# Kernel tuning notes

Measured on AMD Instinct MI355X. Metric: run time of the kernel, lower is better.

The kernel has to match this reference:

```python
import jax, jax.numpy as jnp
import numpy as np

HIDDEN = 1024
N_HEADS = 16
N_KV = 4
HEAD_DIM = HIDDEN // N_HEADS  # 64


def setup_inputs() -> dict:
    key = jax.random.key(0)
    ks = jax.random.split(key, 10)
    B, S, D = 2, 2048, HIDDEN
    s = 0.02
    return {
        "hidden_states": jax.random.normal(ks[0], (B, S, D), jnp.float32),
        "attention_mask": jnp.ones((B, S), jnp.float32),
        "Wq": jax.random.normal(ks[1], (D, N_HEADS * HEAD_DIM), jnp.float32) * s,
        "bq": jnp.zeros((N_HEADS * HEAD_DIM,), jnp.float32),
        "Wk": jax.random.normal(ks[2], (D, N_KV * HEAD_DIM), jnp.float32) * s,
        "bk": jnp.zeros((N_KV * HEAD_DIM,), jnp.float32),
        "Wv": jax.random.normal(ks[3], (D, N_KV * HEAD_DIM), jnp.float32) * s,
        "bv": jnp.zeros((N_KV * HEAD_DIM,), jnp.float32),
        "Wo": jax.random.normal(ks[4], (D, D), jnp.float32) * s,
        "bo": jnp.zeros((D,), jnp.float32),
    }


def _rope(x):
    # x: [B, H, S, Dh]; half-split RoPE as in the torch module
    S, Dh = x.shape[-2], x.shape[-1]
    inv_freq = 1.0 / (10000.0 ** (jnp.arange(0, Dh, 2, dtype=jnp.float32) / Dh))
    freqs = jnp.arange(S, dtype=jnp.float32)[:, None] * inv_freq[None, :]  # [S, Dh/2]
    cos, sin = jnp.cos(freqs), jnp.sin(freqs)
    x1, x2 = jnp.split(x, 2, axis=-1)
    return jnp.concatenate([x1 * cos - x2 * sin, x1 * sin + x2 * cos], axis=-1)


def reference(hidden_states, attention_mask, Wq, bq, Wk, bk, Wv, bv, Wo, bo):
    B, S, D = hidden_states.shape
    q = (hidden_states @ Wq + bq).reshape(B, S, N_HEADS, HEAD_DIM).transpose(0, 2, 1, 3)
    k = (hidden_states @ Wk + bk).reshape(B, S, N_KV, HEAD_DIM).transpose(0, 2, 1, 3)
    v = (hidden_states @ Wv + bv).reshape(B, S, N_KV, HEAD_DIM).transpose(0, 2, 1, 3)
    q = _rope(q)
    k = _rope(k)
    rep = N_HEADS // N_KV
    k = jnp.repeat(k, rep, axis=1)  # [B, H, S, Dh]
    v = jnp.repeat(v, rep, axis=1)
    bias = (1.0 - attention_mask[:, None, None, :]) * -1e9  # [B,1,1,S]
    scores = jnp.einsum("bhqd,bhkd->bhqk", q, k) / jnp.sqrt(jnp.float32(HEAD_DIM))
    attn = jax.nn.softmax(scores + bias, axis=-1)
    out = jnp.einsum("bhqk,bhkd->bhqd", attn, v)
    out = out.transpose(0, 2, 1, 3).reshape(B, S, D)
    return out @ Wo + bo
```

## Files before the change

### kernel.cpp

```cpp
#include <hip/hip_runtime.h>

typedef __bf16 bf16;
typedef __attribute__((ext_vector_type(8))) __bf16 bf16x8;
typedef __attribute__((ext_vector_type(4))) __bf16 bf16x4;
typedef __attribute__((ext_vector_type(4))) float f32x4;
typedef __attribute__((ext_vector_type(16))) float f32x16;
typedef __attribute__((ext_vector_type(4))) unsigned int uint4v;

#define LOG2E 1.44269504088896340736f
#define QSCALE 0.18033688011112042f

__device__ inline void tr_tile(const float* __restrict__ in, bf16* __restrict__ out,
                               int R, int C, int bx, int by, int tid) {
    __shared__ float t[32][33];
    int tx = tid & 31, ty = tid >> 5;
    int rbase = by * 32, cbase = bx * 32;
#pragma unroll
    for (int i = 0; i < 4; i++) {
        int r = ty + i * 8;
        t[r][tx] = in[(size_t)(rbase + r) * C + cbase + tx];
    }
    __syncthreads();
#pragma unroll
    for (int i = 0; i < 4; i++) {
        int r = ty + i * 8;
        out[(size_t)(cbase + r) * R + rbase + tx] = (bf16)t[tx][r];
    }
}

__global__ __launch_bounds__(256) void prep_k(const float* __restrict__ X,
                                              const float* __restrict__ Wq,
                                              const float* __restrict__ Wk,
                                              const float* __restrict__ Wv,
                                              const float* __restrict__ Wo,
                                              const float* __restrict__ mask,
                                              bf16* __restrict__ Xb,
                                              bf16* __restrict__ WqT,
                                              bf16* __restrict__ WkT,
                                              bf16* __restrict__ WvT,
                                              bf16* __restrict__ WoT,
                                              float2* __restrict__ rt,
                                              float* __restrict__ Mb,
                                              int* __restrict__ mflags) {
    int blk = blockIdx.x, tid = threadIdx.x;
    if (blk < 2048) {
        int idx = (blk * 256 + tid) * 8;
        float4 a = *(const float4*)(X + idx);
        float4 b = *(const float4*)(X + idx + 4);
        bf16 v[8] = {(bf16)a.x, (bf16)a.y, (bf16)a.z, (bf16)a.w,
                     (bf16)b.x, (bf16)b.y, (bf16)b.z, (bf16)b.w};
        *(uint4*)(Xb + idx) = *(const uint4*)v;
    } else if (blk < 3072) {
        int t = blk - 2048; tr_tile(Wq, WqT, 1024, 1024, t & 31, t >> 5, tid);
    } else if (blk < 3328) {
        int t = blk - 3072; tr_tile(Wk, WkT, 1024, 256, t & 7, t >> 3, tid);
    } else if (blk < 3584) {
        int t = blk - 3328; tr_tile(Wv, WvT, 1024, 256, t & 7, t >> 3, tid);
    } else if (blk < 4608) {
        int t = blk - 3584; tr_tile(Wo, WoT, 1024, 1024, t & 31, t >> 5, tid);
    } else if (blk < 4864) {
        int idx = (blk - 4608) * 256 + tid;
        int s = idx >> 5, i = idx & 31;
        float inv = exp2f(-0.41524100370589830f * (float)i);
        float ang = (float)s * inv;
        rt[idx] = make_float2(cosf(ang), sinf(ang));
    } else {
        __shared__ int sflag;
        int b = blk - 4864;
        if (tid == 0) sflag = 1;
        __syncthreads();
        const float* mrow = mask + (size_t)b * 2048;
        int i0 = tid * 8;
        bool ones = true;
#pragma unroll
        for (int j = 0; j < 8; j++) {
            float m = mrow[i0 + j];
            if (m != 1.0f) ones = false;
            Mb[(size_t)b * 2048 + i0 + j] = (1.0f - m) * (-1e9f) * LOG2E;
        }
        if (!ones) sflag = 0;
        __syncthreads();
        if (tid == 0) mflags[b] = sflag;
    }
}

__global__ __launch_bounds__(256) void vtrans_k(const unsigned short* __restrict__ in,
                                                unsigned short* __restrict__ out) {
    __shared__ unsigned short t[32][33];
    int z = blockIdx.z;
    const unsigned short* ip = in + (size_t)z * 2048 * 64;
    unsigned short* op = out + (size_t)z * 2048 * 64;
    int tx = threadIdx.x & 31, ty = threadIdx.x >> 5;
    int rbase = blockIdx.y * 32, cbase = blockIdx.x * 32;
#pragma unroll
    for (int i = 0; i < 4; i++) {
        int r = ty + i * 8;
        t[r][tx] = ip[(size_t)(rbase + r) * 64 + cbase + tx];
    }
    __syncthreads();
#pragma unroll
    for (int i = 0; i < 4; i++) {
        int r = ty + i * 8;
        op[(size_t)(cbase + r) * 2048 + rbase + tx] = t[tx][r];
    }
}

__device__ __forceinline__ void gemm_main_12864(const bf16* __restrict__ A,
                                                const bf16* __restrict__ BT,
                                                int m0, int n0, int tid,
                                                f32x4 (&acc)[2][4]) {
    __shared__ bf16 As[128 * 64];
    __shared__ bf16 Bs[64 * 64];
    int w = tid >> 6, lane = tid & 63, l15 = lane & 15, quad = lane >> 4;

    int srow = lane >> 3;
    int kx = ((lane & 7) ^ srow) * 8;
    const bf16* ga0 = A + (size_t)(m0 + w * 32 + srow) * 1024 + kx;
    const bf16* gb0 = BT + (size_t)(n0 + w * 16 + srow) * 1024 + kx;
    bf16* la0 = As + (w * 32) * 64 + lane * 8;
    bf16* lb0 = Bs + (w * 16) * 64 + lane * 8;

    for (int k0 = 0; k0 < 1024; k0 += 64) {
#pragma unroll
        for (int p = 0; p < 4; p++)
            __builtin_amdgcn_global_load_lds(
                (const __attribute__((address_space(1))) unsigned int*)(ga0 + (size_t)p * 8 * 1024 + k0),
                (__attribute__((address_space(3))) unsigned int*)(la0 + p * 512), 16, 0, 0);
#pragma unroll
        for (int p = 0; p < 2; p++)
            __builtin_amdgcn_global_load_lds(
                (const __attribute__((address_space(1))) unsigned int*)(gb0 + (size_t)p * 8 * 1024 + k0),
                (__attribute__((address_space(3))) unsigned int*)(lb0 + p * 512), 16, 0, 0);
        __syncthreads();
#pragma unroll
        for (int half = 0; half < 2; half++) {
            bf16x8 a[2], bfr[4];
            int kp = ((half * 4 + quad) ^ (l15 & 7)) * 8;
#pragma unroll
            for (int i = 0; i < 2; i++)
                a[i] = *(const bf16x8*)&As[(w * 32 + i * 16 + l15) * 64 + kp];
#pragma unroll
            for (int j = 0; j < 4; j++)
                bfr[j] = *(const bf16x8*)&Bs[(j * 16 + l15) * 64 + kp];
#pragma unroll
            for (int i = 0; i < 2; i++)
#pragma unroll
                for (int j = 0; j < 4; j++)
                    acc[i][j] = __builtin_amdgcn_mfma_f32_16x16x32_bf16(a[i], bfr[j], acc[i][j], 0, 0, 0);
        }
        __syncthreads();
    }
}

__global__ __launch_bounds__(256) void qkv_gemm2(const bf16* __restrict__ Xb,
                                                 const bf16* __restrict__ WTall,
                                                 const float* __restrict__ bq,
                                                 const float* __restrict__ bk,
                                                 const float* __restrict__ bv,
                                                 const float2* __restrict__ rt,
                                                 bf16* __restrict__ Qb,
                                                 bf16* __restrict__ Kb,
                                                 bf16* __restrict__ Vb) {
    int tt = blockIdx.x, gy = blockIdx.y, tid = threadIdx.x;
    f32x4 acc[2][4] = {};
    gemm_main_12864(Xb, WTall, tt * 128, gy * 64, tid, acc);

    int w = tid >> 6, lane = tid & 63, l15 = lane & 15, quad = lane >> 4;
    const float* bias;
    bf16* dst;
    int mode, head;
    if (gy < 16)      { head = gy;      bias = bq + head * 64; dst = Qb; mode = 0; }
    else if (gy < 20) { head = gy - 16; bias = bk + head * 64; dst = Kb; mode = 1; }
    else              { head = gy - 20; bias = bv + head * 64; dst = Vb; mode = 2; }

#pragma unroll
    for (int i = 0; i < 2; i++) {
#pragma unroll
        for (int r = 0; r < 4; r++) {
            int token = tt * 128 + w * 32 + i * 16 + quad * 4 + r;
            int b = token >> 11, s = token & 2047;
            float vals[4];
#pragma unroll
            for (int j = 0; j < 4; j++) vals[j] = acc[i][j][r] + bias[j * 16 + l15];
            if (mode <= 1) {
#pragma unroll
                for (int c = 0; c < 2; c++) {
                    float2 cs2 = rt[s * 32 + c * 16 + l15];
                    float x1 = vals[c], x2 = vals[c + 2];
                    vals[c]     = x1 * cs2.x - x2 * cs2.y;
                    vals[c + 2] = x1 * cs2.y + x2 * cs2.x;
                }
            }
            if (mode == 0) {
#pragma unroll
                for (int j = 0; j < 4; j++) vals[j] *= QSCALE;
            }
            size_t base;
            if (mode == 0) base = (((size_t)b * 16 + head) * 2048 + s) * 64;
            else           base = (((size_t)b * 4  + head) * 2048 + s) * 64;
#pragma unroll
            for (int j = 0; j < 4; j++) dst[base + j * 16 + l15] = (bf16)vals[j];
        }
    }
}

__global__ __launch_bounds__(256) void oproj_gemm2(const bf16* __restrict__ Ab,
                                                   const bf16* __restrict__ WoT,
                                                   const float* __restrict__ bo,
                                                   float* __restrict__ out) {
    int tt = blockIdx.x, nt = blockIdx.y, tid = threadIdx.x;
    f32x4 acc[2][4] = {};
    gemm_main_12864(Ab, WoT, tt * 128, nt * 64, tid, acc);

    int w = tid >> 6, lane = tid & 63, l15 = lane & 15, quad = lane >> 4;
#pragma unroll
    for (int i = 0; i < 2; i++) {
#pragma unroll
        for (int r = 0; r < 4; r++) {
            int token = tt * 128 + w * 32 + i * 16 + quad * 4 + r;
#pragma unroll
            for (int j = 0; j < 4; j++) {
                int n = nt * 64 + j * 16 + l15;
                out[(size_t)token * 1024 + n] = acc[i][j][r] + bo[n];
            }
        }
    }
}

__global__ __launch_bounds__(256, 4) void attn_k(const bf16* __restrict__ Qb,
                                                 const bf16* __restrict__ Kb,
                                                 const bf16* __restrict__ VbT,
                                                 const float* __restrict__ Mb,
                                                 const int* __restrict__ mflags,
                                                 bf16* __restrict__ Opb,
                                                 float* __restrict__ Lp) {
    int qt = blockIdx.x, h = blockIdx.y, z = blockIdx.z;
    int b = z >> 1, sp = z & 1;
    int kvh = h >> 2;
    int kt0 = sp * 16;

    __shared__ bf16 Ks[2][64 * 64];
    __shared__ bf16 Vs[2][64 * 64];

    int tid = threadIdx.x, w = tid >> 6, lane = tid & 63, l31 = lane & 31, hi = lane >> 5;

    const bool maskOnes = (mflags[b] != 0);

    bf16x8 qa[4];
    {
        size_t qrow = (((size_t)b * 16 + h) * 2048 + (size_t)qt * 128 + w * 32 + l31) * 64;
#pragma unroll
        for (int ds = 0; ds < 4; ds++)
            qa[ds] = *(const bf16x8*)(Qb + qrow + ds * 16 + hi * 8);
    }

    f32x16 oacc[2] = {};
    float lsum = 0.f;

    size_t kRow = ((size_t)b * 4 + kvh) * 2048;
    size_t vRow = ((size_t)b * 4 + kvh) * 64;

    int srow = lane >> 3;
    int kx = ((lane & 7) ^ srow) * 8;
    const bf16* gk0 = Kb + (kRow + w * 16 + srow) * 64 + kx;
    const bf16* gv0 = VbT + (vRow + w * 16 + srow) * 2048 + kx;
    int lofs = (w * 16) * 64 + lane * 8;

#define STAGE(KT, BUF)                                                                              \
    do {                                                                                            \
        _Pragma("unroll")                                                                           \
        for (int p = 0; p < 2; p++) {                                                               \
            __builtin_amdgcn_global_load_lds(                                                       \
                (const __attribute__((address_space(1))) unsigned int*)(gk0 + ((size_t)(KT) * 64 + p * 8) * 64), \
                (__attribute__((address_space(3))) unsigned int*)(&Ks[BUF][0] + lofs + p * 512), 16, 0, 0); \
            __builtin_amdgcn_global_load_lds(                                                       \
                (const __attribute__((address_space(1))) unsigned int*)(gv0 + (size_t)p * 8 * 2048 + (KT) * 64), \
                (__attribute__((address_space(3))) unsigned int*)(&Vs[BUF][0] + lofs + p * 512), 16, 0, 0); \
        }                                                                                           \
    } while (0)

    STAGE(kt0, 0);
    __syncthreads();

    const float* mbase = Mb + (size_t)b * 2048 + hi * 4;

    for (int kt = 0; kt < 16; kt++) {
        int cb = kt & 1;
        if (kt < 15) STAGE(kt0 + kt + 1, cb ^ 1);
        int ktg = kt0 + kt;

        const bf16* ksb = &Ks[cb][0];
        const bf16* vsb = &Vs[cb][0];

        uint4v paw[4];
#pragma unroll
        for (int kh = 0; kh < 2; kh++) {
            bf16x8 ka[4];
#pragma unroll
            for (int ds = 0; ds < 4; ds++) {
                int gran = ((ds * 2 + hi) ^ (l31 & 7)) * 8;
                ka[ds] = *(const bf16x8*)&ksb[(kh * 32 + l31) * 64 + gran];
            }
            f32x16 s = {};
#pragma unroll
            for (int ds = 0; ds < 4; ds++)
                s = __builtin_amdgcn_mfma_f32_32x32x16_bf16(ka[ds], qa[ds], s, 0, 0, 0);
            if (!maskOnes) {
#pragma unroll
                for (int g = 0; g < 4; g++) {
                    f32x4 b4 = *(const f32x4*)(mbase + ktg * 64 + kh * 32 + g * 8);
#pragma unroll
                    for (int r = 0; r < 4; r++) s[g * 4 + r] += b4[r];
                }
            }
#pragma unroll
            for (int i = 0; i < 16; i++) { s[i] = exp2f(s[i]); lsum += s[i]; }
            unsigned int d0, d1, d2, d3, d4, d5, d6, d7;
            asm("v_cvt_pk_bf16_f32 %0, %1, %2" : "=v"(d0) : "v"(s[0]),  "v"(s[1]));
            asm("v_cvt_pk_bf16_f32 %0, %1, %2" : "=v"(d1) : "v"(s[2]),  "v"(s[3]));
            asm("v_cvt_pk_bf16_f32 %0, %1, %2" : "=v"(d2) : "v"(s[4]),  "v"(s[5]));
            asm("v_cvt_pk_bf16_f32 %0, %1, %2" : "=v"(d3) : "v"(s[6]),  "v"(s[7]));
            asm("v_cvt_pk_bf16_f32 %0, %1, %2" : "=v"(d4) : "v"(s[8]),  "v"(s[9]));
            asm("v_cvt_pk_bf16_f32 %0, %1, %2" : "=v"(d5) : "v"(s[10]), "v"(s[11]));
            asm("v_cvt_pk_bf16_f32 %0, %1, %2" : "=v"(d6) : "v"(s[12]), "v"(s[13]));
            asm("v_cvt_pk_bf16_f32 %0, %1, %2" : "=v"(d7) : "v"(s[14]), "v"(s[15]));
            asm("v_permlane32_swap_b32 %0, %1" : "+v"(d0), "+v"(d2));
            asm("v_permlane32_swap_b32 %0, %1" : "+v"(d1), "+v"(d3));
            asm("v_permlane32_swap_b32 %0, %1" : "+v"(d4), "+v"(d6));
            asm("v_permlane32_swap_b32 %0, %1" : "+v"(d5), "+v"(d7));
            paw[kh * 2 + 0][0] = d0; paw[kh * 2 + 0][1] = d1;
            paw[kh * 2 + 0][2] = d2; paw[kh * 2 + 0][3] = d3;
            paw[kh * 2 + 1][0] = d4; paw[kh * 2 + 1][1] = d5;
            paw[kh * 2 + 1][2] = d6; paw[kh * 2 + 1][3] = d7;
        }

#pragma unroll
        for (int dg = 0; dg < 2; dg++)
#pragma unroll
            for (int ks = 0; ks < 4; ks++) {
                int gran = ((ks * 2 + hi) ^ (l31 & 7)) * 8;
                bf16x8 vb = *(const bf16x8*)&vsb[(dg * 32 + l31) * 64 + gran];
                oacc[dg] = __builtin_amdgcn_mfma_f32_32x32x16_bf16(
                    __builtin_bit_cast(bf16x8, paw[ks]), vb, oacc[dg], 0, 0, 0);
            }
        __syncthreads();
    }
#undef STAGE

    lsum += __shfl_xor(lsum, 32, 64);

#pragma unroll
    for (int dg = 0; dg < 2; dg++)
#pragma unroll
        for (int reg = 0; reg < 16; reg++) {
            int q = qt * 128 + w * 32 + (reg & 3) + 8 * (reg >> 2) + 4 * hi;
            Opb[((size_t)sp * 4096 + (size_t)b * 2048 + q) * 1024 + h * 64 + dg * 32 + l31] =
                (bf16)oacc[dg][reg];
        }
    if (hi == 0)
        Lp[((size_t)(sp * 2 + b) * 16 + h) * 2048 + qt * 128 + w * 32 + l31] = lsum;
}

__global__ __launch_bounds__(256) void merge_k(const bf16* __restrict__ Opb,
                                               const float* __restrict__ Lp,
                                               bf16* __restrict__ Ab) {
    int idx = (blockIdx.x * 256 + threadIdx.x) * 8;
    int tok = idx >> 10;
    int col = idx & 1023;
    int h = col >> 6;
    int b = tok >> 11, q = tok & 2047;
    float l0 = Lp[((size_t)b * 16 + h) * 2048 + q];
    float l1 = Lp[((size_t)(2 + b) * 16 + h) * 2048 + q];
    float inv = 1.0f / (l0 + l1);
    bf16x8 a = *(const bf16x8*)(Opb + idx);
    bf16x8 c = *(const bf16x8*)(Opb + (size_t)4096 * 1024 + idx);
    bf16 o[8];
#pragma unroll
    for (int j = 0; j < 8; j++) o[j] = (bf16)(((float)a[j] + (float)c[j]) * inv);
    *(uint4*)(Ab + idx) = *(const uint4*)o;
}

extern "C" void kernel_launch(void* const* d_in, const int* in_sizes, int n_in,
                              void* d_out, int out_size, void* d_ws, size_t ws_size,
                              hipStream_t stream) {
    const float* X    = (const float*)d_in[0];
    const float* mask = (const float*)d_in[1];
    const float* Wq   = (const float*)d_in[2];
    const float* bq   = (const float*)d_in[3];
    const float* Wk   = (const float*)d_in[4];
    const float* bk   = (const float*)d_in[5];
    const float* Wv   = (const float*)d_in[6];
    const float* bv   = (const float*)d_in[7];
    const float* Wo   = (const float*)d_in[8];
    const float* bo   = (const float*)d_in[9];
    float* out = (float*)d_out;
    bf16* ws  = (bf16*)d_ws;

    bf16* Xb  = ws;
    bf16* WqT = Xb + (size_t)4096 * 1024;
    bf16* WkT = WqT + 1024 * 1024;
    bf16* WvT = WkT + 256 * 1024;
    bf16* WoT = WvT + 256 * 1024;
    bf16* Qb  = WoT + 1024 * 1024;
    bf16* Kb  = Qb + (size_t)2 * 16 * 2048 * 64;
    bf16* Vb  = Kb + (size_t)2 * 4 * 2048 * 64;
    bf16* Ab  = Vb + (size_t)2 * 4 * 2048 * 64;
    float2* rt = (float2*)(Ab + (size_t)2 * 2048 * 1024);
    float* Mb  = (float*)(rt + 2048 * 32);
    int* mflags = (int*)(Mb + 2 * 2048);
    bf16* Opb = (bf16*)(mflags + 4);
    float* Lp = (float*)(Opb + (size_t)2 * 4096 * 1024);
    bf16* VbT = Xb;

    prep_k<<<4866, 256, 0, stream>>>(X, Wq, Wk, Wv, Wo, mask, Xb, WqT, WkT, WvT, WoT, rt, Mb, mflags);
    qkv_gemm2<<<dim3(32, 24), 256, 0, stream>>>(Xb, WqT, bq, bk, bv, rt, Qb, Kb, Vb);
    vtrans_k<<<dim3(2, 64, 8), 256, 0, stream>>>((const unsigned short*)Vb, (unsigned short*)VbT);
    attn_k<<<dim3(16, 16, 4), 256, 0, stream>>>(Qb, Kb, VbT, Mb, mflags, Opb, Lp);
    merge_k<<<2048, 256, 0, stream>>>(Opb, Lp, Ab);
    oproj_gemm2<<<dim3(32, 16), 256, 0, stream>>>(Ab, WoT, bo, out);
}
```

Baseline: 186.7 us.

## Double-buffer GEMM LDS staging and fuse V transpose into QKV epilogue

The shared GEMM mainloop now uses two LDS buffers, issuing global-to-LDS loads for the next k-slice before computing on the current one, so there is one barrier per step instead of two. The QKV kernel's V tiles are transposed through LDS in the epilogue and written directly as VbT with 16-byte stores, which removes the separate vtrans kernel launch and its extra pass over memory. LDS use per block doubles to 48KB, which may limit occupancy.

```diff
diff --git a/kernel.cpp b/kernel.cpp
--- a/kernel.cpp
+++ b/kernel.cpp
@@ -84,54 +84,43 @@
     }
 }
 
-__global__ __launch_bounds__(256) void vtrans_k(const unsigned short* __restrict__ in,
-                                                unsigned short* __restrict__ out) {
-    __shared__ unsigned short t[32][33];
-    int z = blockIdx.z;
-    const unsigned short* ip = in + (size_t)z * 2048 * 64;
-    unsigned short* op = out + (size_t)z * 2048 * 64;
-    int tx = threadIdx.x & 31, ty = threadIdx.x >> 5;
-    int rbase = blockIdx.y * 32, cbase = blockIdx.x * 32;
-#pragma unroll
-    for (int i = 0; i < 4; i++) {
-        int r = ty + i * 8;
-        t[r][tx] = ip[(size_t)(rbase + r) * 64 + cbase + tx];
-    }
-    __syncthreads();
-#pragma unroll
-    for (int i = 0; i < 4; i++) {
-        int r = ty + i * 8;
-        op[(size_t)(cbase + r) * 2048 + rbase + tx] = t[tx][r];
-    }
-}
-
-__device__ __forceinline__ void gemm_main_12864(const bf16* __restrict__ A,
-                                                const bf16* __restrict__ BT,
-                                                int m0, int n0, int tid,
-                                                f32x4 (&acc)[2][4]) {
-    __shared__ bf16 As[128 * 64];
-    __shared__ bf16 Bs[64 * 64];
+__device__ __forceinline__ void gemm_main_db(bf16* __restrict__ pool,
+                                             const bf16* __restrict__ A,
+                                             const bf16* __restrict__ BT,
+                                             int m0, int n0, int tid,
+                                             f32x4 (&acc)[2][4]) {
     int w = tid >> 6, lane = tid & 63, l15 = lane & 15, quad = lane >> 4;
 
     int srow = lane >> 3;
     int kx = ((lane & 7) ^ srow) * 8;
     const bf16* ga0 = A + (size_t)(m0 + w * 32 + srow) * 1024 + kx;
     const bf16* gb0 = BT + (size_t)(n0 + w * 16 + srow) * 1024 + kx;
-    bf16* la0 = As + (w * 32) * 64 + lane * 8;
-    bf16* lb0 = Bs + (w * 16) * 64 + lane * 8;
-
-    for (int k0 = 0; k0 < 1024; k0 += 64) {
-#pragma unroll
-        for (int p = 0; p < 4; p++)
-            __builtin_amdgcn_global_load_lds(
-                (const __attribute__((address_space(1))) unsigned int*)(ga0 + (size_t)p * 8 * 1024 + k0),
-                (__attribute__((address_space(3))) unsigned int*)(la0 + p * 512), 16, 0, 0);
-#pragma unroll
-        for (int p = 0; p < 2; p++)
-            __builtin_amdgcn_global_load_lds(
-                (const __attribute__((address_space(1))) unsigned int*)(gb0 + (size_t)p * 8 * 1024 + k0),
-                (__attribute__((address_space(3))) unsigned int*)(lb0 + p * 512), 16, 0, 0);
-        __syncthreads();
+    int laofs = (w * 32) * 64 + lane * 8;
+    int lbofs = 128 * 64 + (w * 16) * 64 + lane * 8;
+
+#define GSTAGE(K0, BUF)                                                                             \
+    do {                                                                                            \
+        bf16* gbase = pool + (BUF) * 12288;                                                         \
+        _Pragma("unroll")                                                                           \
+        for (int p = 0; p < 4; p++)                                                                 \
+            __builtin_amdgcn_global_load_lds(                                                       \
+                (const __attribute__((address_space(1))) unsigned int*)(ga0 + (size_t)p * 8 * 1024 + (K0)), \
+                (__attribute__((address_space(3))) unsigned int*)(gbase + laofs + p * 512), 16, 0, 0); \
+        _Pragma("unroll")                                                                           \
+        for (int p = 0; p < 2; p++)                                                                 \
+            __builtin_amdgcn_global_load_lds(                                                       \
+                (const __attribute__((address_space(1))) unsigned int*)(gb0 + (size_t)p * 8 * 1024 + (K0)), \
+                (__attribute__((address_space(3))) unsigned int*)(gbase + lbofs + p * 512), 16, 0, 0); \
+    } while (0)
+
+    GSTAGE(0, 0);
+    __syncthreads();
+
+    for (int ks = 0; ks < 16; ks++) {
+        int cb = ks & 1;
+        if (ks < 15) GSTAGE((ks + 1) * 64, cb ^ 1);
+        const bf16* As = pool + cb * 12288;
+        const bf16* Bs = As + 128 * 64;
 #pragma unroll
         for (int half = 0; half < 2; half++) {
             bf16x8 a[2], bfr[4];
@@ -150,6 +139,7 @@
         }
         __syncthreads();
     }
+#undef GSTAGE
 }
 
 __global__ __launch_bounds__(256) void qkv_gemm2(const bf16* __restrict__ Xb,
@@ -160,18 +150,45 @@
                                                  const float2* __restrict__ rt,
                                                  bf16* __restrict__ Qb,
                                                  bf16* __restrict__ Kb,
-                                                 bf16* __restrict__ Vb) {
+                                                 bf16* __restrict__ VbT) {
+    __shared__ __align__(16) bf16 pool[2 * 12288];
     int tt = blockIdx.x, gy = blockIdx.y, tid = threadIdx.x;
     f32x4 acc[2][4] = {};
-    gemm_main_12864(Xb, WTall, tt * 128, gy * 64, tid, acc);
+    gemm_main_db(pool, Xb, WTall, tt * 128, gy * 64, tid, acc);
 
     int w = tid >> 6, lane = tid & 63, l15 = lane & 15, quad = lane >> 4;
+
+    if (gy >= 20) {
+        int kvh = gy - 20;
+        const float* bias = bv + kvh * 64;
+        bf16* T = pool;
+#pragma unroll
+        for (int i = 0; i < 2; i++)
+#pragma unroll
+            for (int r = 0; r < 4; r++) {
+                int s_local = w * 32 + i * 16 + quad * 4 + r;
+#pragma unroll
+                for (int j = 0; j < 4; j++) {
+                    int d = j * 16 + l15;
+                    T[d * 136 + s_local] = (bf16)(acc[i][j][r] + bias[d]);
+                }
+            }
+        __syncthreads();
+        int d = tid & 63, sblk = tid >> 6;
+        int b = tt >> 4, s_base = (tt & 15) * 128 + sblk * 32;
+        const bf16* Trow = T + d * 136 + sblk * 32;
+        size_t orow = ((size_t)(b * 4 + kvh) * 64 + d) * 2048 + s_base;
+#pragma unroll
+        for (int c = 0; c < 4; c++)
+            *(uint4*)(VbT + orow + c * 8) = *(const uint4*)(Trow + c * 8);
+        return;
+    }
+
     const float* bias;
     bf16* dst;
     int mode, head;
-    if (gy < 16)      { head = gy;      bias = bq + head * 64; dst = Qb; mode = 0; }
-    else if (gy < 20) { head = gy - 16; bias = bk + head * 64; dst = Kb; mode = 1; }
-    else              { head = gy - 20; bias = bv + head * 64; dst = Vb; mode = 2; }
+    if (gy < 16) { head = gy;      bias = bq + head * 64; dst = Qb; mode = 0; }
+    else         { head = gy - 16; bias = bk + head * 64; dst = Kb; mode = 1; }
 
 #pragma unroll
     for (int i = 0; i < 2; i++) {
@@ -182,14 +199,12 @@
             float vals[4];
 #pragma unroll
             for (int j = 0; j < 4; j++) vals[j] = acc[i][j][r] + bias[j * 16 + l15];
-            if (mode <= 1) {
-#pragma unroll
-                for (int c = 0; c < 2; c++) {
-                    float2 cs2 = rt[s * 32 + c * 16 + l15];
-                    float x1 = vals[c], x2 = vals[c + 2];
-                    vals[c]     = x1 * cs2.x - x2 * cs2.y;
-                    vals[c + 2] = x1 * cs2.y + x2 * cs2.x;
-                }
+#pragma unroll
+            for (int c = 0; c < 2; c++) {
+                float2 cs2 = rt[s * 32 + c * 16 + l15];
+                float x1 = vals[c], x2 = vals[c + 2];
+                vals[c]     = x1 * cs2.x - x2 * cs2.y;
+                vals[c + 2] = x1 * cs2.y + x2 * cs2.x;
             }
             if (mode == 0) {
 #pragma unroll
@@ -208,9 +223,10 @@
                                                    const bf16* __restrict__ WoT,
                                                    const float* __restrict__ bo,
                                                    float* __restrict__ out) {
+    __shared__ __align__(16) bf16 pool[2 * 12288];
     int tt = blockIdx.x, nt = blockIdx.y, tid = threadIdx.x;
     f32x4 acc[2][4] = {};
-    gemm_main_12864(Ab, WoT, tt * 128, nt * 64, tid, acc);
+    gemm_main_db(pool, Ab, WoT, tt * 128, nt * 64, tid, acc);
 
     int w = tid >> 6, lane = tid & 63, l15 = lane & 15, quad = lane >> 4;
 #pragma unroll
@@ -403,18 +419,16 @@
     bf16* WoT = WvT + 256 * 1024;
     bf16* Qb  = WoT + 1024 * 1024;
     bf16* Kb  = Qb + (size_t)2 * 16 * 2048 * 64;
-    bf16* Vb  = Kb + (size_t)2 * 4 * 2048 * 64;
-    bf16* Ab  = Vb + (size_t)2 * 4 * 2048 * 64;
+    bf16* VbT = Kb + (size_t)2 * 4 * 2048 * 64;
+    bf16* Ab  = VbT + (size_t)2 * 4 * 2048 * 64;
     float2* rt = (float2*)(Ab + (size_t)2 * 2048 * 1024);
     float* Mb  = (float*)(rt + 2048 * 32);
     int* mflags = (int*)(Mb + 2 * 2048);
     bf16* Opb = (bf16*)(mflags + 4);
     float* Lp = (float*)(Opb + (size_t)2 * 4096 * 1024);
-    bf16* VbT = Xb;
 
     prep_k<<<4866, 256, 0, stream>>>(X, Wq, Wk, Wv, Wo, mask, Xb, WqT, WkT, WvT, WoT, rt, Mb, mflags);
-    qkv_gemm2<<<dim3(32, 24), 256, 0, stream>>>(Xb, WqT, bq, bk, bv, rt, Qb, Kb, Vb);
-    vtrans_k<<<dim3(2, 64, 8), 256, 0, stream>>>((const unsigned short*)Vb, (unsigned short*)VbT);
+    qkv_gemm2<<<dim3(32, 24), 256, 0, stream>>>(Xb, WqT, bq, bk, bv, rt, Qb, Kb, VbT);
     attn_k<<<dim3(16, 16, 4), 256, 0, stream>>>(Qb, Kb, VbT, Mb, mflags, Opb, Lp);
     merge_k<<<2048, 256, 0, stream>>>(Opb, Lp, Ab);
     oproj_gemm2<<<dim3(32, 16), 256, 0, stream>>>(Ab, WoT, bo, out);
```

Result: faster. 180.6 us (-3.2%).
